# Kernel optimization log

Hardware: AMD Instinct MI355X
Metric: run time of the kernel (lower is better)

The kernel has to match this reference:

```python
import jax, jax.numpy as jnp
import numpy as np

B, S, E, H = 32, 2048, 512, 512


def setup_inputs() -> dict:
    key = jax.random.key(0)
    ks = jax.random.split(key, 6)
    scale = 1.0 / np.sqrt(H)  # PyTorch LSTM init range
    x = jax.random.normal(ks[0], (B, S, E), dtype=jnp.float32)
    lengths = jax.random.randint(ks[1], (B,), 1, S + 1, dtype=jnp.int32)
    W_ih = jax.random.uniform(ks[2], (4 * H, E), jnp.float32, -scale, scale)
    W_hh = jax.random.uniform(ks[3], (4 * H, H), jnp.float32, -scale, scale)
    b_ih = jax.random.uniform(ks[4], (4 * H,), jnp.float32, -scale, scale)
    b_hh = jax.random.uniform(ks[5], (4 * H,), jnp.float32, -scale, scale)
    return {"x": x, "lengths": lengths, "W_ih": W_ih, "W_hh": W_hh,
            "b_ih": b_ih, "b_hh": b_hh}


def _lstm_scan(x, W_ih, W_hh, b_ih, b_hh):
    # x: [B, S, E]. Precompute input projections for all timesteps (one big GEMM).
    x_proj = jnp.einsum('bse,ge->bsg', x, W_ih) + (b_ih + b_hh)  # [B, S, 4H]
    x_proj_t = jnp.swapaxes(x_proj, 0, 1)  # [S, B, 4H]

    def step(carry, xp_t):
        h, c = carry
        gates = xp_t + h @ W_hh.T  # [B, 4H]
        i, f, g, o = jnp.split(gates, 4, axis=-1)  # PyTorch gate order i,f,g,o
        i = jax.nn.sigmoid(i)
        f = jax.nn.sigmoid(f)
        g = jnp.tanh(g)
        o = jax.nn.sigmoid(o)
        c = f * c + i * g
        h = o * jnp.tanh(c)
        return (h, c), h

    h0 = jnp.zeros((B, H), dtype=x.dtype)
    c0 = jnp.zeros((B, H), dtype=x.dtype)
    (_, _), hs = jax.lax.scan(step, (h0, c0), x_proj_t)  # hs: [S, B, H]
    return hs


def reference(x, lengths, W_ih, W_hh, b_ih, b_hh):
    hs = _lstm_scan(x, W_ih, W_hh, b_ih, b_hh)  # [S, B, H]
    # zero-mask outputs at positions >= length (matches __maskLSTMOutput)
    mask = (jnp.arange(S)[:, None] < lengths[None, :]).astype(hs.dtype)  # [S, B]
    out = (hs * mask[:, :, None]).transpose(1, 0, 2)[:, :, None, :]  # [B, S, 1, H]
    # hidden state captured at t = length-1 per sequence (matches __updateHiddenOutput)
    hidden = hs[lengths - 1, jnp.arange(B)][None, :, :]  # [1, B, H]
    return (out, lengths, hidden)
```

## Files before the change

### kernel.cpp

```cpp
#include <hip/hip_runtime.h>


typedef __attribute__((ext_vector_type(8))) __bf16 bf16x8;
typedef __attribute__((ext_vector_type(8))) short short8;
typedef __attribute__((ext_vector_type(4))) float floatx4;

#define XP_OFF   0ull
#define XP_BYTES (2048ull * 32ull * 2048ull * 2ull)
#define HPK_OFF  (XP_OFF + XP_BYTES)
#define HPK_BYTES (2ull * 16384ull * 4ull)
#define BIAS_OFF (HPK_OFF + HPK_BYTES)
#define FLAG_OFF (BIAS_OFF + 8192ull)
#define WS_NEED  (FLAG_OFF + 256ull)

#define LEN_OFF_F    33554432
#define HIDDEN_OFF_F 33554464

__device__ inline float sigm(float x) { return 1.f / (1.f + __expf(-x)); }
__device__ inline float tanh_(float x) {
  float e = __expf(-2.f * fabsf(x));
  float r = (1.f - e) / (1.f + e);
  return x >= 0.f ? r : -r;
}

__device__ inline void cvt_hilo8(const float* v, bf16x8& hi, bf16x8& lo) {
#pragma unroll
  for (int i = 0; i < 8; ++i) {
    __bf16 h = (__bf16)v[i];
    hi[i] = h;
    lo[i] = (__bf16)(v[i] - (float)h);
  }
}

__device__ inline float bf16f(unsigned short u) {
  union { unsigned u; float f; } c; c.u = ((unsigned)u) << 16; return c.f;
}

__global__ __launch_bounds__(256) void prep_kernel(
    const float* __restrict__ bih, const float* __restrict__ bhh,
    const int* __restrict__ len, float* __restrict__ biasp,
    unsigned* __restrict__ hpk, unsigned* __restrict__ flags,
    float* __restrict__ outf) {
  const int tid = threadIdx.x;
  for (int i = tid; i < 2048; i += 256) {
    int rowg = (i & 3) * 512 + (i >> 4) * 4 + ((i >> 2) & 3);
    biasp[i] = bih[rowg] + bhh[rowg];
  }
  for (int i = tid; i < 32768; i += 256) hpk[i] = 0u;
  if (tid < 64) flags[tid] = 0u;
  if (tid < 32) outf[LEN_OFF_F + tid] = (float)len[tid];
}

__global__ __launch_bounds__(256) void xproj_gemm(
    const float* __restrict__ x, const float* __restrict__ Wih,
    const float* __restrict__ biasp, __bf16* __restrict__ xp) {
  __shared__ short Ash[64 * 40], Asl[64 * 40], Bsh[64 * 40], Bsl[64 * 40];
  const int tid = threadIdx.x;
  const int w = tid >> 6, lane = tid & 63, ln = lane & 15, kq = lane >> 4;
  const int ntile = blockIdx.x & 31, mtile = blockIdx.x >> 5;
  const int srow = tid >> 2, sseg = tid & 3;

  const size_t a_base = (size_t)(mtile * 64 + srow) * 512 + sseg * 8;
  const int np_s = ntile * 64 + srow;
  const int rowg = (np_s & 3) * 512 + (np_s >> 4) * 4 + ((np_s >> 2) & 3);
  const size_t b_base = (size_t)rowg * 512 + sseg * 8;

  floatx4 acc[4] = {{0,0,0,0},{0,0,0,0},{0,0,0,0},{0,0,0,0}};

  for (int k0 = 0; k0 < 512; k0 += 32) {
    floatx4 a0 = *(const floatx4*)(x + a_base + k0);
    floatx4 a1 = *(const floatx4*)(x + a_base + k0 + 4);
    floatx4 b0 = *(const floatx4*)(Wih + b_base + k0);
    floatx4 b1 = *(const floatx4*)(Wih + b_base + k0 + 4);
    __syncthreads();
    {
      float va[8] = {a0[0],a0[1],a0[2],a0[3],a1[0],a1[1],a1[2],a1[3]};
      bf16x8 hi, lo; cvt_hilo8(va, hi, lo);
      *(short8*)&Ash[srow * 40 + sseg * 8] = __builtin_bit_cast(short8, hi);
      *(short8*)&Asl[srow * 40 + sseg * 8] = __builtin_bit_cast(short8, lo);
      float vb[8] = {b0[0],b0[1],b0[2],b0[3],b1[0],b1[1],b1[2],b1[3]};
      cvt_hilo8(vb, hi, lo);
      *(short8*)&Bsh[srow * 40 + sseg * 8] = __builtin_bit_cast(short8, hi);
      *(short8*)&Bsl[srow * 40 + sseg * 8] = __builtin_bit_cast(short8, lo);
    }
    __syncthreads();
    bf16x8 ah = __builtin_bit_cast(bf16x8, *(const short8*)&Ash[(16 * w + ln) * 40 + kq * 8]);
    bf16x8 al = __builtin_bit_cast(bf16x8, *(const short8*)&Asl[(16 * w + ln) * 40 + kq * 8]);
#pragma unroll
    for (int nt = 0; nt < 4; ++nt) {
      bf16x8 bh = __builtin_bit_cast(bf16x8, *(const short8*)&Bsh[(nt * 16 + ln) * 40 + kq * 8]);
      bf16x8 bl = __builtin_bit_cast(bf16x8, *(const short8*)&Bsl[(nt * 16 + ln) * 40 + kq * 8]);
      acc[nt] = __builtin_amdgcn_mfma_f32_16x16x32_bf16(ah, bh, acc[nt], 0, 0, 0);
      acc[nt] = __builtin_amdgcn_mfma_f32_16x16x32_bf16(al, bh, acc[nt], 0, 0, 0);
      acc[nt] = __builtin_amdgcn_mfma_f32_16x16x32_bf16(ah, bl, acc[nt], 0, 0, 0);
    }
  }
#pragma unroll
  for (int nt = 0; nt < 4; ++nt) {
    const int npg = ntile * 64 + nt * 16 + ln;
    const float bs = biasp[npg];
#pragma unroll
    for (int r = 0; r < 4; ++r) {
      const int m = mtile * 64 + w * 16 + kq * 4 + r;
      const int s = m & 2047, b = m >> 11;
      xp[(size_t)(s * 32 + b) * 2048 + npg] = (__bf16)(acc[nt][r] + bs);
    }
  }
}

__global__ __launch_bounds__(256, 1) void lstm_rec(
    const float* __restrict__ Whh, const int* __restrict__ lengths,
    const __bf16* __restrict__ xp, float* __restrict__ out,
    float* __restrict__ hid, unsigned* __restrict__ hpk,
    unsigned* __restrict__ flags) {
  __shared__ short Hh[16 * 512];
  __shared__ short Hl[16 * 512];
  __shared__ float Part[4 * 1088];

  const int tid = threadIdx.x;
  const int w = tid >> 6, lane = tid & 63, ln = lane & 15, kq = lane >> 4;
  const int bh = blockIdx.x >> 5;
  const int ug = blockIdx.x & 31;
  const int b0 = bh * 16;

  bf16x8 whi[4][4], wlo[4][4];
#pragma unroll
  for (int nt = 0; nt < 4; ++nt) {
    const int rowg = (ln & 3) * 512 + (ug * 4 + nt) * 4 + (ln >> 2);
#pragma unroll
    for (int kc = 0; kc < 4; ++kc) {
      const int k = w * 128 + kc * 32 + kq * 8;
      floatx4 f0 = *(const floatx4*)(Whh + (size_t)rowg * 512 + k);
      floatx4 f1 = *(const floatx4*)(Whh + (size_t)rowg * 512 + k + 4);
      float v[8] = {f0[0],f0[1],f0[2],f0[3],f1[0],f1[1],f1[2],f1[3]};
      cvt_hilo8(v, whi[nt][kc], wlo[nt][kc]);
    }
  }

  const int m_e = tid >> 4, ue = tid & 15;
  const int b_e = b0 + m_e, u_e = ug * 16 + ue;
  const int lenb = lengths[b_e];
  float cst = 0.f, hcap = 0.f;

  const __bf16* xpb = xp + (size_t)b_e * 2048 + ug * 64 + (ue >> 2) * 16 + (ue & 3) * 4;
  unsigned long long xpcur =
      __builtin_nontemporal_load((const unsigned long long*)xpb);
  unsigned long long xpnext;

  unsigned* myflag = flags + bh * 32 + ug;
  const unsigned* pollp = flags + bh * 32 + (lane & 31);

  for (int t = 0; t < 2048; ++t) {
    if (w == 0 && t > 0) {
      for (;;) {
        unsigned f = __hip_atomic_load(pollp, __ATOMIC_RELAXED,
                                       __HIP_MEMORY_SCOPE_AGENT);
        if (__ballot(f < (unsigned)t) == 0ull) break;
        __builtin_amdgcn_s_sleep(1);
      }
    }
    __syncthreads();
    const unsigned* src = hpk + (t & 1) * 16384 + b0 * 512;
    unsigned long long v[16];
#pragma unroll
    for (int k = 0; k < 16; ++k)
      v[k] = __hip_atomic_load(
          (const unsigned long long*)(src + k * 512 + tid * 2),
          __ATOMIC_RELAXED, __HIP_MEMORY_SCOPE_AGENT);
    {
      const int g = tid >> 2;
#pragma unroll
      for (int k = 0; k < 16; ++k) {
        const unsigned w0 = (unsigned)v[k], w1 = (unsigned)(v[k] >> 32);
        const int d = k * 512 + ((g ^ (k & 7)) * 8) + (tid & 3) * 2;
        *(unsigned*)&Hh[d] = (w0 >> 16) | (w1 & 0xffff0000u);
        *(unsigned*)&Hl[d] = (w0 & 0xffffu) | (w1 << 16);
      }
    }
    __syncthreads();
    floatx4 acc[4] = {{0,0,0,0},{0,0,0,0},{0,0,0,0},{0,0,0,0}};
#pragma unroll
    for (int kc = 0; kc < 4; ++kc) {
      const int g = w * 16 + kc * 4 + kq;
      const int d = ln * 512 + ((g ^ (ln & 7)) * 8);
      bf16x8 ah = __builtin_bit_cast(bf16x8, *(const short8*)&Hh[d]);
      bf16x8 al = __builtin_bit_cast(bf16x8, *(const short8*)&Hl[d]);
#pragma unroll
      for (int nt = 0; nt < 4; ++nt) {
        acc[nt] = __builtin_amdgcn_mfma_f32_16x16x32_bf16(ah, whi[nt][kc], acc[nt], 0, 0, 0);
        acc[nt] = __builtin_amdgcn_mfma_f32_16x16x32_bf16(al, whi[nt][kc], acc[nt], 0, 0, 0);
        acc[nt] = __builtin_amdgcn_mfma_f32_16x16x32_bf16(ah, wlo[nt][kc], acc[nt], 0, 0, 0);
      }
    }
#pragma unroll
    for (int nt = 0; nt < 4; ++nt)
#pragma unroll
      for (int r4 = 0; r4 < 4; ++r4)
        Part[w * 1088 + nt * 272 + (kq * 4 + r4) * 16 + ln] = acc[nt][r4];
    __syncthreads();
    {
      const int pb = (ue >> 2) * 272 + m_e * 16 + (ue & 3) * 4;
      floatx4 p0 = *(const floatx4*)&Part[pb];
      floatx4 p1 = *(const floatx4*)&Part[1088 + pb];
      floatx4 p2 = *(const floatx4*)&Part[2176 + pb];
      floatx4 p3 = *(const floatx4*)&Part[3264 + pb];
      const float xg0 = bf16f((unsigned short)(xpcur & 0xffffu));
      const float xg1 = bf16f((unsigned short)((xpcur >> 16) & 0xffffu));
      const float xg2 = bf16f((unsigned short)((xpcur >> 32) & 0xffffu));
      const float xg3 = bf16f((unsigned short)(xpcur >> 48));
      const float pi = xg0 + p0[0] + p1[0] + p2[0] + p3[0];
      const float pf = xg1 + p0[1] + p1[1] + p2[1] + p3[1];
      const float pg = xg2 + p0[2] + p1[2] + p2[2] + p3[2];
      const float po = xg3 + p0[3] + p1[3] + p2[3] + p3[3];
      const float gi_ = sigm(pi), gf = sigm(pf), gg = tanh_(pg), go = sigm(po);
      cst = gf * cst + gi_ * gg;
      const float hv = go * tanh_(cst);
      const __bf16 hb = (__bf16)hv;
      const __bf16 lb = (__bf16)(hv - (float)hb);
      const unsigned pk =
          ((unsigned)__builtin_bit_cast(unsigned short, hb) << 16) |
          (unsigned)__builtin_bit_cast(unsigned short, lb);
      __hip_atomic_store(hpk + ((t + 1) & 1) * 16384 + b_e * 512 + u_e, pk,
                         __ATOMIC_RELAXED, __HIP_MEMORY_SCOPE_AGENT);
      asm volatile("s_waitcnt vmcnt(0)" ::: "memory");
      __syncthreads();
      if (tid == 0)
        __hip_atomic_store(myflag, (unsigned)(t + 1), __ATOMIC_RELAXED,
                           __HIP_MEMORY_SCOPE_AGENT);
      __builtin_nontemporal_store((t < lenb) ? hv : 0.f,
                                  &out[((size_t)b_e * 2048 + t) * 512 + u_e]);
      if (t == lenb - 1) hcap = hv;
    }
    {
      const int tn = (t + 1 < 2048) ? t + 1 : 2047;
      xpnext = __builtin_nontemporal_load(
          (const unsigned long long*)(xpb + (size_t)tn * 65536));
    }
    xpcur = xpnext;
  }
  hid[b_e * 512 + u_e] = hcap;
}

extern "C" void kernel_launch(void* const* d_in, const int* in_sizes, int n_in,
                              void* d_out, int out_size, void* d_ws, size_t ws_size,
                              hipStream_t stream) {
  const float* x = (const float*)d_in[0];
  const int* lengths = (const int*)d_in[1];
  const float* Wih = (const float*)d_in[2];
  const float* Whh = (const float*)d_in[3];
  const float* bih = (const float*)d_in[4];
  const float* bhh = (const float*)d_in[5];
  float* outf = (float*)d_out;
  char* ws = (char*)d_ws;
  if (ws_size < WS_NEED) return;

  float* biasp = (float*)(ws + BIAS_OFF);
  __bf16* xp = (__bf16*)(ws + XP_OFF);
  unsigned* hpk = (unsigned*)(ws + HPK_OFF);
  unsigned* flags = (unsigned*)(ws + FLAG_OFF);

  prep_kernel<<<1, 256, 0, stream>>>(bih, bhh, lengths, biasp, hpk, flags, outf);
  xproj_gemm<<<32768, 256, 0, stream>>>(x, Wih, biasp, xp);
  lstm_rec<<<64, 256, 0, stream>>>(Whh, lengths, xp, outf,
                                   outf + HIDDEN_OFF_F, hpk, flags);
}
```

Baseline: 7.092 ms.

## Replace per-block flag barrier with step-tagged hidden-state entries polled directly

Each hidden-state value is now published as a 64-bit entry that carries the timestep tag beside the packed hi/lo bf16 pair. Consumers spin on the data itself until every entry they need carries the current step. This removes the separate flag store, the vmcnt wait and one block barrier before the flag, plus the flag-poll round trip and a barrier on the consumer side. In exchange the exchange buffer doubles in size, every thread polls 32 words instead of one wave polling flags, and correctness now relies on 64-bit atomic stores being single-copy atomic.

```diff
diff --git a/kernel.cpp b/kernel.cpp
--- a/kernel.cpp
+++ b/kernel.cpp
@@ -5,13 +5,12 @@
 typedef __attribute__((ext_vector_type(8))) short short8;
 typedef __attribute__((ext_vector_type(4))) float floatx4;
 
-#define XP_OFF   0ull
-#define XP_BYTES (2048ull * 32ull * 2048ull * 2ull)
-#define HPK_OFF  (XP_OFF + XP_BYTES)
-#define HPK_BYTES (2ull * 16384ull * 4ull)
-#define BIAS_OFF (HPK_OFF + HPK_BYTES)
-#define FLAG_OFF (BIAS_OFF + 8192ull)
-#define WS_NEED  (FLAG_OFF + 256ull)
+#define XP_OFF    0ull
+#define XP_BYTES  (2048ull * 32ull * 2048ull * 2ull)
+#define ENT_OFF   (XP_OFF + XP_BYTES)
+#define ENT_BYTES (2ull * 32ull * 512ull * 8ull)
+#define BIAS_OFF  (ENT_OFF + ENT_BYTES)
+#define WS_NEED   (BIAS_OFF + 8192ull)
 
 #define LEN_OFF_F    33554432
 #define HIDDEN_OFF_F 33554464
@@ -39,16 +38,14 @@
 __global__ __launch_bounds__(256) void prep_kernel(
     const float* __restrict__ bih, const float* __restrict__ bhh,
     const int* __restrict__ len, float* __restrict__ biasp,
-    unsigned* __restrict__ hpk, unsigned* __restrict__ flags,
-    float* __restrict__ outf) {
-  const int tid = threadIdx.x;
-  for (int i = tid; i < 2048; i += 256) {
-    int rowg = (i & 3) * 512 + (i >> 4) * 4 + ((i >> 2) & 3);
-    biasp[i] = bih[rowg] + bhh[rowg];
-  }
-  for (int i = tid; i < 32768; i += 256) hpk[i] = 0u;
-  if (tid < 64) flags[tid] = 0u;
-  if (tid < 32) outf[LEN_OFF_F + tid] = (float)len[tid];
+    unsigned long long* __restrict__ ent, float* __restrict__ outf) {
+  const int gtid = blockIdx.x * 256 + threadIdx.x;
+  if (gtid < 2048) {
+    int rowg = (gtid & 3) * 512 + (gtid >> 4) * 4 + ((gtid >> 2) & 3);
+    biasp[gtid] = bih[rowg] + bhh[rowg];
+  }
+  for (int i = gtid; i < 32768; i += 16384) ent[i] = 0ull;
+  if (gtid < 32) outf[LEN_OFF_F + gtid] = (float)len[gtid];
 }
 
 __global__ __launch_bounds__(256) void xproj_gemm(
@@ -111,8 +108,7 @@
 __global__ __launch_bounds__(256, 1) void lstm_rec(
     const float* __restrict__ Whh, const int* __restrict__ lengths,
     const __bf16* __restrict__ xp, float* __restrict__ out,
-    float* __restrict__ hid, unsigned* __restrict__ hpk,
-    unsigned* __restrict__ flags) {
+    float* __restrict__ hid, unsigned long long* __restrict__ ent) {
   __shared__ short Hh[16 * 512];
   __shared__ short Hl[16 * 512];
   __shared__ float Part[4 * 1088];
@@ -147,37 +143,37 @@
       __builtin_nontemporal_load((const unsigned long long*)xpb);
   unsigned long long xpnext;
 
-  unsigned* myflag = flags + bh * 32 + ug;
-  const unsigned* pollp = flags + bh * 32 + (lane & 31);
+  unsigned long long* pub = ent + (size_t)b_e * 512 + u_e;
+  const unsigned long long* sbw = ent + (size_t)b0 * 512 + 128 * w + 2 * lane;
+  const int g0 = 16 * w + (lane >> 2);
+  const int dlo = (lane & 3) * 2;
 
   for (int t = 0; t < 2048; ++t) {
-    if (w == 0 && t > 0) {
-      for (;;) {
-        unsigned f = __hip_atomic_load(pollp, __ATOMIC_RELAXED,
-                                       __HIP_MEMORY_SCOPE_AGENT);
-        if (__ballot(f < (unsigned)t) == 0ull) break;
-        __builtin_amdgcn_s_sleep(1);
+    const unsigned long long* sb = sbw + (size_t)(t & 1) * 16384;
+    unsigned long long e0[16], e1[16];
+    for (;;) {
+      bool ok = true;
+#pragma unroll
+      for (int k = 0; k < 16; ++k) {
+        e0[k] = __hip_atomic_load(sb + (size_t)k * 512, __ATOMIC_RELAXED,
+                                  __HIP_MEMORY_SCOPE_AGENT);
+        e1[k] = __hip_atomic_load(sb + (size_t)k * 512 + 1, __ATOMIC_RELAXED,
+                                  __HIP_MEMORY_SCOPE_AGENT);
       }
-    }
-    __syncthreads();
-    const unsigned* src = hpk + (t & 1) * 16384 + b0 * 512;
-    unsigned long long v[16];
-#pragma unroll
-    for (int k = 0; k < 16; ++k)
-      v[k] = __hip_atomic_load(
-          (const unsigned long long*)(src + k * 512 + tid * 2),
-          __ATOMIC_RELAXED, __HIP_MEMORY_SCOPE_AGENT);
-    {
-      const int g = tid >> 2;
-#pragma unroll
-      for (int k = 0; k < 16; ++k) {
-        const unsigned w0 = (unsigned)v[k], w1 = (unsigned)(v[k] >> 32);
-        const int d = k * 512 + ((g ^ (k & 7)) * 8) + (tid & 3) * 2;
-        *(unsigned*)&Hh[d] = (w0 >> 16) | (w1 & 0xffff0000u);
-        *(unsigned*)&Hl[d] = (w0 & 0xffffu) | (w1 << 16);
-      }
-    }
-    __syncthreads();
+#pragma unroll
+      for (int k = 0; k < 16; ++k)
+        ok = ok && ((unsigned)(e0[k] >> 32) == (unsigned)t) &&
+             ((unsigned)(e1[k] >> 32) == (unsigned)t);
+      if (__ballot(!ok) == 0ull) break;
+      __builtin_amdgcn_s_sleep(1);
+    }
+#pragma unroll
+    for (int k = 0; k < 16; ++k) {
+      const unsigned w0 = (unsigned)e0[k], w1 = (unsigned)e1[k];
+      const int d = k * 512 + ((g0 ^ (k & 7)) * 8) + dlo;
+      *(unsigned*)&Hh[d] = (w0 >> 16) | (w1 & 0xffff0000u);
+      *(unsigned*)&Hl[d] = (w0 & 0xffffu) | (w1 << 16);
+    }
     floatx4 acc[4] = {{0,0,0,0},{0,0,0,0},{0,0,0,0},{0,0,0,0}};
 #pragma unroll
     for (int kc = 0; kc < 4; ++kc) {
@@ -220,17 +216,15 @@
       const unsigned pk =
           ((unsigned)__builtin_bit_cast(unsigned short, hb) << 16) |
           (unsigned)__builtin_bit_cast(unsigned short, lb);
-      __hip_atomic_store(hpk + ((t + 1) & 1) * 16384 + b_e * 512 + u_e, pk,
+      __hip_atomic_store(pub + (size_t)((t + 1) & 1) * 16384,
+                         ((unsigned long long)(unsigned)(t + 1) << 32) |
+                             (unsigned long long)pk,
                          __ATOMIC_RELAXED, __HIP_MEMORY_SCOPE_AGENT);
-      asm volatile("s_waitcnt vmcnt(0)" ::: "memory");
-      __syncthreads();
-      if (tid == 0)
-        __hip_atomic_store(myflag, (unsigned)(t + 1), __ATOMIC_RELAXED,
-                           __HIP_MEMORY_SCOPE_AGENT);
       __builtin_nontemporal_store((t < lenb) ? hv : 0.f,
                                   &out[((size_t)b_e * 2048 + t) * 512 + u_e]);
       if (t == lenb - 1) hcap = hv;
     }
+    __syncthreads();
     {
       const int tn = (t + 1 < 2048) ? t + 1 : 2047;
       xpnext = __builtin_nontemporal_load(
@@ -256,11 +250,10 @@
 
   float* biasp = (float*)(ws + BIAS_OFF);
   __bf16* xp = (__bf16*)(ws + XP_OFF);
-  unsigned* hpk = (unsigned*)(ws + HPK_OFF);
-  unsigned* flags = (unsigned*)(ws + FLAG_OFF);
-
-  prep_kernel<<<1, 256, 0, stream>>>(bih, bhh, lengths, biasp, hpk, flags, outf);
+  unsigned long long* ent = (unsigned long long*)(ws + ENT_OFF);
+
+  prep_kernel<<<64, 256, 0, stream>>>(bih, bhh, lengths, biasp, ent, outf);
   xproj_gemm<<<32768, 256, 0, stream>>>(x, Wih, biasp, xp);
   lstm_rec<<<64, 256, 0, stream>>>(Whh, lengths, xp, outf,
-                                   outf + HIDDEN_OFF_F, hpk, flags);
-}
+                                   outf + HIDDEN_OFF_F, ent);
+}
```

Result: slower. 8.715 ms (+22.9%).

## Use 32 larger recurrent blocks with per-wave h loads and fewer barriers

Applied to the files above, without the earlier changes.

The recurrent LSTM kernel goes from 64 blocks of 256 threads to 32 blocks of 512 threads. Each block now covers 32 hidden units, split over 8 waves that each handle a 64-wide K slice. Every wave polls 16 flags itself and loads its own slice of h straight into shared memory, which removes two block-wide barriers per timestep and halves the number of blocks taking part in the cross-block handshake. In exchange the partial-sum reduction in shared memory grows to 8 waves, and per-block MFMA work doubles.

```diff
diff --git a/kernel.cpp b/kernel.cpp
--- a/kernel.cpp
+++ b/kernel.cpp
@@ -11,7 +11,7 @@
 #define HPK_BYTES (2ull * 16384ull * 4ull)
 #define BIAS_OFF (HPK_OFF + HPK_BYTES)
 #define FLAG_OFF (BIAS_OFF + 8192ull)
-#define WS_NEED  (FLAG_OFF + 256ull)
+#define WS_NEED  (FLAG_OFF + 128ull)
 
 #define LEN_OFF_F    33554432
 #define HIDDEN_OFF_F 33554464
@@ -47,7 +47,7 @@
     biasp[i] = bih[rowg] + bhh[rowg];
   }
   for (int i = tid; i < 32768; i += 256) hpk[i] = 0u;
-  if (tid < 64) flags[tid] = 0u;
+  if (tid < 32) flags[tid] = 0u;
   if (tid < 32) outf[LEN_OFF_F + tid] = (float)len[tid];
 }
 
@@ -108,28 +108,28 @@
   }
 }
 
-__global__ __launch_bounds__(256, 1) void lstm_rec(
+__global__ __launch_bounds__(512, 2) void lstm_rec(
     const float* __restrict__ Whh, const int* __restrict__ lengths,
     const __bf16* __restrict__ xp, float* __restrict__ out,
     float* __restrict__ hid, unsigned* __restrict__ hpk,
     unsigned* __restrict__ flags) {
   __shared__ short Hh[16 * 512];
   __shared__ short Hl[16 * 512];
-  __shared__ float Part[4 * 1088];
+  __shared__ float Part[8 * 2176];
 
   const int tid = threadIdx.x;
   const int w = tid >> 6, lane = tid & 63, ln = lane & 15, kq = lane >> 4;
-  const int bh = blockIdx.x >> 5;
-  const int ug = blockIdx.x & 31;
+  const int bh = blockIdx.x >> 4;
+  const int ug = blockIdx.x & 15;
   const int b0 = bh * 16;
 
-  bf16x8 whi[4][4], wlo[4][4];
-#pragma unroll
-  for (int nt = 0; nt < 4; ++nt) {
-    const int rowg = (ln & 3) * 512 + (ug * 4 + nt) * 4 + (ln >> 2);
-#pragma unroll
-    for (int kc = 0; kc < 4; ++kc) {
-      const int k = w * 128 + kc * 32 + kq * 8;
+  bf16x8 whi[8][2], wlo[8][2];
+#pragma unroll
+  for (int nt = 0; nt < 8; ++nt) {
+    const int rowg = (ln & 3) * 512 + ug * 32 + nt * 4 + (ln >> 2);
+#pragma unroll
+    for (int kc = 0; kc < 2; ++kc) {
+      const int k = w * 64 + kc * 32 + kq * 8;
       floatx4 f0 = *(const floatx4*)(Whh + (size_t)rowg * 512 + k);
       floatx4 f1 = *(const floatx4*)(Whh + (size_t)rowg * 512 + k + 4);
       float v[8] = {f0[0],f0[1],f0[2],f0[3],f1[0],f1[1],f1[2],f1[3]};
@@ -137,82 +137,85 @@
     }
   }
 
-  const int m_e = tid >> 4, ue = tid & 15;
-  const int b_e = b0 + m_e, u_e = ug * 16 + ue;
+  const int m_e = tid >> 5, ue = tid & 31;
+  const int b_e = b0 + m_e, u_e = ug * 32 + ue;
   const int lenb = lengths[b_e];
   float cst = 0.f, hcap = 0.f;
 
-  const __bf16* xpb = xp + (size_t)b_e * 2048 + ug * 64 + (ue >> 2) * 16 + (ue & 3) * 4;
+  const __bf16* xpb =
+      xp + (size_t)b_e * 2048 + (u_e >> 2) * 16 + (u_e & 3) * 4;
   unsigned long long xpcur =
       __builtin_nontemporal_load((const unsigned long long*)xpb);
   unsigned long long xpnext;
 
-  unsigned* myflag = flags + bh * 32 + ug;
-  const unsigned* pollp = flags + bh * 32 + (lane & 31);
+  unsigned* myflag = flags + bh * 16 + ug;
+  const unsigned* pollp = flags + bh * 16 + (lane & 15);
+
+  const int u0 = w * 64 + 2 * (lane & 31);
+  const int bst = 8 * (lane >> 5);
+  const int gstg = u0 >> 3;
 
   for (int t = 0; t < 2048; ++t) {
-    if (w == 0 && t > 0) {
+    if (t > 0) {
       for (;;) {
-        unsigned f = __hip_atomic_load(pollp, __ATOMIC_RELAXED,
-                                       __HIP_MEMORY_SCOPE_AGENT);
+        unsigned f = (lane < 16)
+                         ? __hip_atomic_load(pollp, __ATOMIC_RELAXED,
+                                             __HIP_MEMORY_SCOPE_AGENT)
+                         : (unsigned)t;
         if (__ballot(f < (unsigned)t) == 0ull) break;
         __builtin_amdgcn_s_sleep(1);
       }
     }
-    __syncthreads();
-    const unsigned* src = hpk + (t & 1) * 16384 + b0 * 512;
-    unsigned long long v[16];
-#pragma unroll
-    for (int k = 0; k < 16; ++k)
-      v[k] = __hip_atomic_load(
-          (const unsigned long long*)(src + k * 512 + tid * 2),
-          __ATOMIC_RELAXED, __HIP_MEMORY_SCOPE_AGENT);
-    {
-      const int g = tid >> 2;
-#pragma unroll
-      for (int k = 0; k < 16; ++k) {
-        const unsigned w0 = (unsigned)v[k], w1 = (unsigned)(v[k] >> 32);
-        const int d = k * 512 + ((g ^ (k & 7)) * 8) + (tid & 3) * 2;
-        *(unsigned*)&Hh[d] = (w0 >> 16) | (w1 & 0xffff0000u);
-        *(unsigned*)&Hl[d] = (w0 & 0xffffu) | (w1 << 16);
-      }
-    }
-    __syncthreads();
-    floatx4 acc[4] = {{0,0,0,0},{0,0,0,0},{0,0,0,0},{0,0,0,0}};
-#pragma unroll
-    for (int kc = 0; kc < 4; ++kc) {
-      const int g = w * 16 + kc * 4 + kq;
+    const unsigned long long* sb = (const unsigned long long*)(
+        hpk + (size_t)(t & 1) * 16384 + (size_t)(b0 + bst) * 512 + u0);
+    unsigned long long e[8];
+#pragma unroll
+    for (int j = 0; j < 8; ++j)
+      e[j] = __hip_atomic_load(sb + (size_t)j * 256, __ATOMIC_RELAXED,
+                               __HIP_MEMORY_SCOPE_AGENT);
+#pragma unroll
+    for (int j = 0; j < 8; ++j) {
+      const int k = bst + j;
+      const unsigned w0 = (unsigned)e[j], w1 = (unsigned)(e[j] >> 32);
+      const int d = k * 512 + ((gstg ^ (k & 7)) * 8) + (u0 & 7);
+      *(unsigned*)&Hh[d] = (w0 >> 16) | (w1 & 0xffff0000u);
+      *(unsigned*)&Hl[d] = (w0 & 0xffffu) | (w1 << 16);
+    }
+    floatx4 acc[8] = {{0,0,0,0},{0,0,0,0},{0,0,0,0},{0,0,0,0},
+                      {0,0,0,0},{0,0,0,0},{0,0,0,0},{0,0,0,0}};
+#pragma unroll
+    for (int kc = 0; kc < 2; ++kc) {
+      const int g = 8 * w + kc * 4 + kq;
       const int d = ln * 512 + ((g ^ (ln & 7)) * 8);
       bf16x8 ah = __builtin_bit_cast(bf16x8, *(const short8*)&Hh[d]);
       bf16x8 al = __builtin_bit_cast(bf16x8, *(const short8*)&Hl[d]);
 #pragma unroll
-      for (int nt = 0; nt < 4; ++nt) {
+      for (int nt = 0; nt < 8; ++nt) {
         acc[nt] = __builtin_amdgcn_mfma_f32_16x16x32_bf16(ah, whi[nt][kc], acc[nt], 0, 0, 0);
         acc[nt] = __builtin_amdgcn_mfma_f32_16x16x32_bf16(al, whi[nt][kc], acc[nt], 0, 0, 0);
         acc[nt] = __builtin_amdgcn_mfma_f32_16x16x32_bf16(ah, wlo[nt][kc], acc[nt], 0, 0, 0);
       }
     }
 #pragma unroll
-    for (int nt = 0; nt < 4; ++nt)
+    for (int nt = 0; nt < 8; ++nt)
 #pragma unroll
       for (int r4 = 0; r4 < 4; ++r4)
-        Part[w * 1088 + nt * 272 + (kq * 4 + r4) * 16 + ln] = acc[nt][r4];
+        Part[(w * 8 + nt) * 272 + (kq * 4 + r4) * 16 + ln] = acc[nt][r4];
     __syncthreads();
     {
       const int pb = (ue >> 2) * 272 + m_e * 16 + (ue & 3) * 4;
-      floatx4 p0 = *(const floatx4*)&Part[pb];
-      floatx4 p1 = *(const floatx4*)&Part[1088 + pb];
-      floatx4 p2 = *(const floatx4*)&Part[2176 + pb];
-      floatx4 p3 = *(const floatx4*)&Part[3264 + pb];
+      float s0 = 0.f, s1 = 0.f, s2 = 0.f, s3 = 0.f;
+#pragma unroll
+      for (int wv = 0; wv < 8; ++wv) {
+        floatx4 p = *(const floatx4*)&Part[wv * 2176 + pb];
+        s0 += p[0]; s1 += p[1]; s2 += p[2]; s3 += p[3];
+      }
       const float xg0 = bf16f((unsigned short)(xpcur & 0xffffu));
       const float xg1 = bf16f((unsigned short)((xpcur >> 16) & 0xffffu));
       const float xg2 = bf16f((unsigned short)((xpcur >> 32) & 0xffffu));
       const float xg3 = bf16f((unsigned short)(xpcur >> 48));
-      const float pi = xg0 + p0[0] + p1[0] + p2[0] + p3[0];
-      const float pf = xg1 + p0[1] + p1[1] + p2[1] + p3[1];
-      const float pg = xg2 + p0[2] + p1[2] + p2[2] + p3[2];
-      const float po = xg3 + p0[3] + p1[3] + p2[3] + p3[3];
-      const float gi_ = sigm(pi), gf = sigm(pf), gg = tanh_(pg), go = sigm(po);
+      const float gi_ = sigm(xg0 + s0), gf = sigm(xg1 + s1);
+      const float gg = tanh_(xg2 + s2), go = sigm(xg3 + s3);
       cst = gf * cst + gi_ * gg;
       const float hv = go * tanh_(cst);
       const __bf16 hb = (__bf16)hv;
@@ -220,8 +223,9 @@
       const unsigned pk =
           ((unsigned)__builtin_bit_cast(unsigned short, hb) << 16) |
           (unsigned)__builtin_bit_cast(unsigned short, lb);
-      __hip_atomic_store(hpk + ((t + 1) & 1) * 16384 + b_e * 512 + u_e, pk,
-                         __ATOMIC_RELAXED, __HIP_MEMORY_SCOPE_AGENT);
+      __hip_atomic_store(hpk + (size_t)((t + 1) & 1) * 16384 +
+                             (size_t)b_e * 512 + u_e,
+                         pk, __ATOMIC_RELAXED, __HIP_MEMORY_SCOPE_AGENT);
       asm volatile("s_waitcnt vmcnt(0)" ::: "memory");
       __syncthreads();
       if (tid == 0)
@@ -261,6 +265,6 @@
 
   prep_kernel<<<1, 256, 0, stream>>>(bih, bhh, lengths, biasp, hpk, flags, outf);
   xproj_gemm<<<32768, 256, 0, stream>>>(x, Wih, biasp, xp);
-  lstm_rec<<<64, 256, 0, stream>>>(Whh, lengths, xp, outf,
+  lstm_rec<<<32, 512, 0, stream>>>(Whh, lengths, xp, outf,
                                    outf + HIDDEN_OFF_F, hpk, flags);
 }
```

After: 8.803 ms. +24.1%, slower.
